# Optimization experiments

Measured on AMD Instinct MI355X. Metric: run time of the kernel, lower is better.

Reference implementation:

```python
import jax, jax.numpy as jnp
import numpy as np

NUM_HEADS = 16
MAX_LEN = 2048


def setup_inputs() -> dict:
    key = jax.random.key(0)
    ks = jax.random.split(key, 10)
    L, B, C = 2048, 2, 1024
    s = 0.02
    return {
        "x": jax.random.normal(ks[0], (L, B, C), dtype=jnp.float32),
        "Wq": jax.random.normal(ks[1], (C, C), dtype=jnp.float32) * s,
        "bq": jnp.zeros((C,), dtype=jnp.float32),
        "Wk": jax.random.normal(ks[2], (C, C), dtype=jnp.float32) * s,
        "bk": jnp.zeros((C,), dtype=jnp.float32),
        "Wv": jax.random.normal(ks[3], (C, C), dtype=jnp.float32) * s,
        "bv": jnp.zeros((C,), dtype=jnp.float32),
        "Wo": jax.random.normal(ks[4], (C, C), dtype=jnp.float32) * s,
        "bo": jnp.zeros((C,), dtype=jnp.float32),
        "rel": jax.random.normal(ks[5], (2 * MAX_LEN - 1,), dtype=jnp.float32) * s,
    }


def reference(x, Wq, bq, Wk, bk, Wv, bv, Wo, bo, rel):
    L, B, C = x.shape
    H = NUM_HEADS
    hd = C // H
    scale = hd ** (-0.5)
    xb = jnp.transpose(x, (1, 0, 2))  # (B, L, C)

    def heads(y):  # (B, L, C) -> (B, H, L, hd)
        return jnp.transpose(y.reshape(B, L, H, hd), (0, 2, 1, 3))

    Q = heads(xb @ Wq + bq)
    K = heads(xb @ Wk + bk)
    V = heads(xb @ Wv + bv)

    scores = jnp.einsum("bhqd,bhkd->bhqk", Q, K)  # (B, H, L, L)
    # relative-position bias gather: offset = k - q + max_len - 1
    idx = jnp.arange(L)[None, :] - jnp.arange(L)[:, None] + (MAX_LEN - 1)
    R = rel[idx]  # (L, L)
    scores = (scores + R[None, None, :, :]) * scale
    w = jax.nn.softmax(scores, axis=-1)
    attn = jnp.einsum("bhqk,bhkd->bhqd", w, V)  # (B, H, L, hd)
    attn = jnp.transpose(attn, (0, 2, 1, 3)).reshape(B, L, C)
    attn = jnp.transpose(attn, (1, 0, 2))  # (L, B, C)
    return attn @ Wo + bo
```

## Files before the change

kernel.cpp:

```cpp
#include <hip/hip_runtime.h>

#define L_SEQ 2048
#define BATCH 2
#define CDIM  1024
#define NH    16
#define HD    64

typedef __attribute__((ext_vector_type(8))) short short8;
typedef __attribute__((ext_vector_type(4))) float floatx4;

#define QSCALE 0.18033688011112042f

__device__ __forceinline__ unsigned short f2bf(float f){
  unsigned int u = __builtin_bit_cast(unsigned int, f);
  u += 0x7fffu + ((u >> 16) & 1u);
  return (unsigned short)(u >> 16);
}

__device__ __forceinline__ void gload_lds16(const void* g, void* l){
  typedef __attribute__((address_space(1))) void gv_t;
  typedef __attribute__((address_space(3))) void sv_t;
  __builtin_amdgcn_global_load_lds((gv_t*)(void*)g, (sv_t*)l, 16, 0, 0);
}

__global__ void __launch_bounds__(256) prep_x(const float* __restrict__ x,
                                              unsigned short* __restrict__ xb){
  int idx = blockIdx.x * 256 + threadIdx.x;
  int c4 = idx & 255;
  int lb = idx >> 8;
  int b  = lb & (BATCH - 1);
  int l  = lb >> 1;
  float4 v = ((const float4*)x)[idx];
  ushort4 s;
  s.x = f2bf(v.x); s.y = f2bf(v.y); s.z = f2bf(v.z); s.w = f2bf(v.w);
  *(ushort4*)&xb[(size_t)(b*L_SEQ + l)*CDIM + c4*4] = s;
}

__global__ void __launch_bounds__(256) prep_w(const float* __restrict__ Wq,
    const float* __restrict__ Wk, const float* __restrict__ Wv,
    const float* __restrict__ Wo, unsigned short* __restrict__ Wqkvt,
    unsigned short* __restrict__ Wot){
  __shared__ float tile[32][33];
  int z = blockIdx.z;
  const float* W = (z==0)?Wq:(z==1)?Wk:(z==2)?Wv:Wo;
  unsigned short* dst = (z==3) ? Wot : (Wqkvt + (size_t)z*CDIM*CDIM);
  int tx = threadIdx.x & 31, ty = threadIdx.x >> 5;
  int X = blockIdx.x*32, Y = blockIdx.y*32;
  #pragma unroll
  for (int i=0;i<4;i++)
    tile[ty + i*8][tx] = W[(size_t)(Y + ty + i*8)*CDIM + X + tx];
  __syncthreads();
  #pragma unroll
  for (int i=0;i<4;i++)
    dst[(size_t)(X + ty + i*8)*CDIM + Y + tx] = f2bf(tile[tx][ty + i*8]);
}

template<int MODE>
__global__ void __launch_bounds__(256) gemm_bt(
    const unsigned short* __restrict__ A,
    const unsigned short* __restrict__ Bt,
    int Kdim,
    const float* __restrict__ b0, const float* __restrict__ b1,
    const float* __restrict__ b2,
    unsigned short* __restrict__ qo, unsigned short* __restrict__ ko,
    unsigned short* __restrict__ vo, float* __restrict__ out)
{
  __shared__ unsigned short Asm[128*32];
  __shared__ unsigned short Bsm[128*32];
  const int t    = threadIdx.x;
  const int lane = t & 63;
  const int wave = t >> 6;
  const int wr = wave >> 1, wc = wave & 1;
  const int g = lane >> 4, lr = lane & 15;
  const int rowA0 = blockIdx.x * 128;
  const int rowB0 = blockIdx.y * 128;

  floatx4 acc[4][4] = {};

  const int r_st = t >> 2;
  const int k_st = (t & 3) * 8;

  for (int k0 = 0; k0 < Kdim; k0 += 32) {
    const unsigned short* ga = A  + (size_t)(rowA0 + r_st) * Kdim + k0 + k_st;
    const unsigned short* gb = Bt + (size_t)(rowB0 + r_st) * Kdim + k0 + k_st;
    gload_lds16(ga,                   &Asm[t*8]);
    gload_lds16(ga + (size_t)64*Kdim, &Asm[2048 + t*8]);
    gload_lds16(gb,                   &Bsm[t*8]);
    gload_lds16(gb + (size_t)64*Kdim, &Bsm[2048 + t*8]);
    __syncthreads();
    short8 af[4], bfr[4];
    #pragma unroll
    for (int mi=0;mi<4;mi++)
      af[mi] = *(const short8*)&Asm[(wr*64 + mi*16 + lr)*32 + g*8];
    #pragma unroll
    for (int ni=0;ni<4;ni++)
      bfr[ni] = *(const short8*)&Bsm[(wc*64 + ni*16 + lr)*32 + g*8];
    #pragma unroll
    for (int mi=0;mi<4;mi++)
      #pragma unroll
      for (int ni=0;ni<4;ni++)
        acc[mi][ni] = __builtin_amdgcn_mfma_f32_16x16x32_bf16(af[mi], bfr[ni], acc[mi][ni], 0, 0, 0);
    __syncthreads();
  }

  #pragma unroll
  for (int mi=0;mi<4;mi++){
    const int rb = rowA0 + wr*64 + mi*16 + g*4;
    #pragma unroll
    for (int ni=0;ni<4;ni++){
      const int col = rowB0 + wc*64 + ni*16 + lr;
      if (MODE == 0) {
        const int sec = col >> 10;
        const int nl  = col & 1023;
        const int h = nl >> 6, d = nl & 63;
        const float* bp = (sec==0) ? b0 : (sec==1) ? b1 : b2;
        const float bias = bp[nl];
        #pragma unroll
        for (int r=0;r<4;r++){
          const int row = rb + r;
          const int b = row >> 11, l = row & 2047;
          float v = acc[mi][ni][r] + bias;
          if (sec == 0) v *= QSCALE;
          const unsigned short hv = f2bf(v);
          const size_t bh = (size_t)(b*NH + h);
          if (sec == 0)      qo[(bh*L_SEQ + l)*HD + d] = hv;
          else if (sec == 1) ko[(bh*L_SEQ + l)*HD + d] = hv;
          else               vo[(bh*HD + d)*L_SEQ + l] = hv;
        }
      } else {
        const float bias = b0[col];
        #pragma unroll
        for (int r=0;r<4;r++){
          const int row = rb + r;
          const int b = row >> 11, l = row & 2047;
          out[((size_t)l*BATCH + b)*CDIM + col] = acc[mi][ni][r] + bias;
        }
      }
    }
  }
}

__global__ void __launch_bounds__(256) attn_kernel(
    const unsigned short* __restrict__ Qb, const unsigned short* __restrict__ Kb,
    const unsigned short* __restrict__ Vt, const float* __restrict__ rel,
    unsigned short* __restrict__ Ab)
{
  __shared__ unsigned short Ks[2][64*64];
  __shared__ unsigned short Vs[2][64*64];
  __shared__ unsigned int Pl[4*16*32];
  const int bh = blockIdx.x;
  const int qb = blockIdx.y;
  const int t = threadIdx.x, lane = t & 63, wave = t >> 6;
  const int g = lane >> 4, lr = lane & 15;

  const unsigned short* Qp = Qb + (size_t)bh * (L_SEQ*HD);
  const unsigned short* Kp = Kb + (size_t)bh * (L_SEQ*HD);
  const unsigned short* Vp = Vt + (size_t)bh * (HD*L_SEQ);

  const int q0 = qb*64 + wave*16;
  const short8 qf0 = *(const short8*)&Qp[(size_t)(q0 + lr)*HD + g*8];
  const short8 qf1 = *(const short8*)&Qp[(size_t)(q0 + lr)*HD + 32 + g*8];

  const float* relp = rel + (2047 - q0 - lr + g*4);

  unsigned int* pw = Pl + wave*512 + lr*32;
  const int swz = lr & 7;

  const int srow = t >> 3;
  const int sxor = (t & 7) ^ (srow & 7);

  const unsigned short* kg = Kp + (size_t)srow*HD + sxor*8;
  const unsigned short* vg = Vp + (size_t)srow*L_SEQ + sxor*8;

  floatx4 o[4] = {};
  float m = -1e30f, lsum = 0.f;

  gload_lds16(kg,           &Ks[0][t*8]);
  gload_lds16(kg + 32*HD,   &Ks[0][2048 + t*8]);
  gload_lds16(vg,           &Vs[0][t*8]);
  gload_lds16(vg + (size_t)32*L_SEQ, &Vs[0][2048 + t*8]);
  __syncthreads();

  int cur = 0;
  for (int kb = 0; kb < L_SEQ; kb += 64) {
    {
      const int kbn = (kb + 64) & (L_SEQ - 1);
      const unsigned short* kgn = kg + (size_t)kbn*HD;
      const unsigned short* vgn = vg + kbn;
      unsigned short* kd = &Ks[cur^1][0];
      unsigned short* vd = &Vs[cur^1][0];
      gload_lds16(kgn,                    kd + t*8);
      gload_lds16(kgn + 32*HD,            kd + 2048 + t*8);
      gload_lds16(vgn,                    vd + t*8);
      gload_lds16(vgn + (size_t)32*L_SEQ, vd + 2048 + t*8);
    }

    float relv[16];
    #pragma unroll
    for (int j=0;j<4;j++)
      #pragma unroll
      for (int r=0;r<4;r++)
        relv[4*j+r] = relp[kb + 16*j + r];

    const unsigned short* kbuf = &Ks[cur][0];
    floatx4 s[4];
    #pragma unroll
    for (int j=0;j<4;j++){
      const int row = j*16 + lr;
      const short8 k0 = *(const short8*)&kbuf[row*64 + ((g    ) ^ swz)*8];
      const short8 k1 = *(const short8*)&kbuf[row*64 + ((4 + g) ^ swz)*8];
      floatx4 z = {};
      z = __builtin_amdgcn_mfma_f32_16x16x32_bf16(k0, qf0, z, 0,0,0);
      z = __builtin_amdgcn_mfma_f32_16x16x32_bf16(k1, qf1, z, 0,0,0);
      s[j] = z;
    }

    float p[16];
    #pragma unroll
    for (int j=0;j<4;j++)
      #pragma unroll
      for (int r=0;r<4;r++)
        p[4*j+r] = fmaf(relv[4*j+r], QSCALE, s[j][r]);

    float ma = fmaxf(fmaxf(fmaxf(p[0],p[1]),fmaxf(p[2],p[3])),
                     fmaxf(fmaxf(p[4],p[5]),fmaxf(p[6],p[7])));
    float mb = fmaxf(fmaxf(fmaxf(p[8],p[9]),fmaxf(p[10],p[11])),
                     fmaxf(fmaxf(p[12],p[13]),fmaxf(p[14],p[15])));
    float mx = fmaxf(ma, mb);
    mx = fmaxf(mx, __shfl_xor(mx, 16, 64));
    mx = fmaxf(mx, __shfl_xor(mx, 32, 64));
    const float mn = fmaxf(m, mx);
    const float al = exp2f(m - mn);
    m = mn;
    #pragma unroll
    for (int i=0;i<16;i++) p[i] = exp2f(p[i] - mn);
    float t0 = (p[0]+p[1]) + (p[2]+p[3]);
    float t1 = (p[4]+p[5]) + (p[6]+p[7]);
    float t2 = (p[8]+p[9]) + (p[10]+p[11]);
    float t3 = (p[12]+p[13]) + (p[14]+p[15]);
    float ss = (t0+t1) + (t2+t3);
    ss += __shfl_xor(ss, 16, 64);
    ss += __shfl_xor(ss, 32, 64);
    lsum = lsum*al + ss;
    #pragma unroll
    for (int fb=0;fb<4;fb++)
      #pragma unroll
      for (int r=0;r<4;r++) o[fb][r] *= al;

    #pragma unroll
    for (int j=0;j<4;j++){
      unsigned lo = (unsigned)f2bf(p[4*j])   | ((unsigned)f2bf(p[4*j+1])<<16);
      unsigned hi = (unsigned)f2bf(p[4*j+2]) | ((unsigned)f2bf(p[4*j+3])<<16);
      const int unit = (2*j + (g>>1)) ^ swz;
      *(uint2*)&pw[unit*4 + (g&1)*2] = make_uint2(lo, hi);
    }
    asm volatile("" ::: "memory");
    const short8 pf0 = *(const short8*)&pw[((    g) ^ swz)*4];
    const short8 pf1 = *(const short8*)&pw[((4 + g) ^ swz)*4];
    asm volatile("" ::: "memory");

    const unsigned short* vbuf = &Vs[cur][0];
    #pragma unroll
    for (int fb=0; fb<4; fb++){
      const int row = fb*16 + lr;
      const short8 v0 = *(const short8*)&vbuf[row*64 + ((g    ) ^ swz)*8];
      const short8 v1 = *(const short8*)&vbuf[row*64 + ((4 + g) ^ swz)*8];
      o[fb] = __builtin_amdgcn_mfma_f32_16x16x32_bf16(v0, pf0, o[fb], 0,0,0);
      o[fb] = __builtin_amdgcn_mfma_f32_16x16x32_bf16(v1, pf1, o[fb], 0,0,0);
    }

    __syncthreads();
    cur ^= 1;
  }

  const float inv = 1.f / lsum;
  const int b = bh >> 4, h = bh & 15;
  unsigned short* outp = &Ab[((size_t)(b*L_SEQ + q0 + lr))*CDIM + h*HD];
  #pragma unroll
  for (int fb=0; fb<4; fb++){
    #pragma unroll
    for (int rp=0; rp<2; rp++){
      const float v0 = o[fb][2*rp]   * inv;
      const float v1 = o[fb][2*rp+1] * inv;
      *(unsigned int*)&outp[fb*16 + g*4 + 2*rp] =
          (unsigned)f2bf(v0) | ((unsigned)f2bf(v1) << 16);
    }
  }
}

extern "C" void kernel_launch(void* const* d_in, const int* in_sizes, int n_in,
                              void* d_out, int out_size, void* d_ws, size_t ws_size,
                              hipStream_t stream) {
  const float* x   = (const float*)d_in[0];
  const float* Wq  = (const float*)d_in[1];
  const float* bq  = (const float*)d_in[2];
  const float* Wk  = (const float*)d_in[3];
  const float* bk  = (const float*)d_in[4];
  const float* Wv  = (const float*)d_in[5];
  const float* bv  = (const float*)d_in[6];
  const float* Wo  = (const float*)d_in[7];
  const float* bo  = (const float*)d_in[8];
  const float* rel = (const float*)d_in[9];
  float* out = (float*)d_out;

  char* ws = (char*)d_ws;
  unsigned short* Xb    = (unsigned short*)(ws);
  unsigned short* Wqkvt = (unsigned short*)(ws + (8u  << 20));
  unsigned short* Wot   = (unsigned short*)(ws + (14u << 20));
  unsigned short* Qb    = (unsigned short*)(ws + (16u << 20));
  unsigned short* Kb    = (unsigned short*)(ws + (24u << 20));
  unsigned short* Vt    = (unsigned short*)(ws + (32u << 20));
  unsigned short* Ab    = Xb;

  prep_x<<<4096, 256, 0, stream>>>(x, Xb);
  prep_w<<<dim3(32,32,4), 256, 0, stream>>>(Wq, Wk, Wv, Wo, Wqkvt, Wot);
  gemm_bt<0><<<dim3(32,24), 256, 0, stream>>>(Xb, Wqkvt, CDIM, bq, bk, bv,
                                              Qb, Kb, Vt, nullptr);
  attn_kernel<<<dim3(32,32), 256, 0, stream>>>(Qb, Kb, Vt, rel, Ab);
  gemm_bt<1><<<dim3(32,8), 256, 0, stream>>>(Ab, Wot, CDIM, bo, nullptr, nullptr,
                                             nullptr, nullptr, nullptr, out);
}
```

Measured before the change: 248.8 us.

## Lazy softmax rescale, MFMA row-sum, and packed bf16 conversion in attention

The online-softmax running max is now updated only when some lane's block max exceeds the stored max by more than a threshold of 8 (in log2 units), so the cross-lane max shuffles and output rescaling are skipped on most iterations. The row-sum reduction is moved onto the matrix cores by multiplying a ones vector with the bf16 probability fragments, which removes the shuffle-based sum. Manual bf16 rounding is replaced with the hardware packed convert instruction. The trade-off is extra MFMA work per iteration, a divergent branch, and a sum taken over bf16-rounded probabilities that can reach up to 2^8 before rescaling.

```diff
diff --git a/kernel.cpp b/kernel.cpp
--- a/kernel.cpp
+++ b/kernel.cpp
@@ -15,6 +15,12 @@
   unsigned int u = __builtin_bit_cast(unsigned int, f);
   u += 0x7fffu + ((u >> 16) & 1u);
   return (unsigned short)(u >> 16);
+}
+
+__device__ __forceinline__ unsigned cvtpk(float lo, float hi){
+  unsigned r;
+  asm("v_cvt_pk_bf16_f32 %0, %1, %2" : "=v"(r) : "v"(lo), "v"(hi));
+  return r;
 }
 
 __device__ __forceinline__ void gload_lds16(const void* g, void* l){
@@ -166,6 +172,9 @@
   unsigned int* pw = Pl + wave*512 + lr*32;
   const int swz = lr & 7;
 
+  const short ONE = (short)0x3F80;
+  const short8 ones = { ONE,ONE,ONE,ONE,ONE,ONE,ONE,ONE };
+
   const int srow = t >> 3;
   const int sxor = (t & 7) ^ (srow & 7);
 
@@ -173,7 +182,8 @@
   const unsigned short* vg = Vp + (size_t)srow*L_SEQ + sxor*8;
 
   floatx4 o[4] = {};
-  float m = -1e30f, lsum = 0.f;
+  floatx4 osum = {};
+  float m = -1e30f;
 
   gload_lds16(kg,           &Ks[0][t*8]);
   gload_lds16(kg + 32*HD,   &Ks[0][2048 + t*8]);
@@ -222,35 +232,32 @@
       for (int r=0;r<4;r++)
         p[4*j+r] = fmaf(relv[4*j+r], QSCALE, s[j][r]);
 
-    float ma = fmaxf(fmaxf(fmaxf(p[0],p[1]),fmaxf(p[2],p[3])),
-                     fmaxf(fmaxf(p[4],p[5]),fmaxf(p[6],p[7])));
-    float mb = fmaxf(fmaxf(fmaxf(p[8],p[9]),fmaxf(p[10],p[11])),
-                     fmaxf(fmaxf(p[12],p[13]),fmaxf(p[14],p[15])));
-    float mx = fmaxf(ma, mb);
-    mx = fmaxf(mx, __shfl_xor(mx, 16, 64));
-    mx = fmaxf(mx, __shfl_xor(mx, 32, 64));
-    const float mn = fmaxf(m, mx);
-    const float al = exp2f(m - mn);
-    m = mn;
-    #pragma unroll
-    for (int i=0;i<16;i++) p[i] = exp2f(p[i] - mn);
-    float t0 = (p[0]+p[1]) + (p[2]+p[3]);
-    float t1 = (p[4]+p[5]) + (p[6]+p[7]);
-    float t2 = (p[8]+p[9]) + (p[10]+p[11]);
-    float t3 = (p[12]+p[13]) + (p[14]+p[15]);
-    float ss = (t0+t1) + (t2+t3);
-    ss += __shfl_xor(ss, 16, 64);
-    ss += __shfl_xor(ss, 32, 64);
-    lsum = lsum*al + ss;
-    #pragma unroll
-    for (int fb=0;fb<4;fb++)
-      #pragma unroll
-      for (int r=0;r<4;r++) o[fb][r] *= al;
+    float ma = fmaxf(fmaxf(fmaxf(p[0],p[1]),p[2]),  fmaxf(fmaxf(p[3],p[4]),p[5]));
+    float mb = fmaxf(fmaxf(fmaxf(p[6],p[7]),p[8]),  fmaxf(fmaxf(p[9],p[10]),p[11]));
+    float mc = fmaxf(fmaxf(fmaxf(p[12],p[13]),p[14]), p[15]);
+    float mxl = fmaxf(fmaxf(ma, mb), mc);
+
+    if (!__all(mxl <= m + 8.f)) {
+      float mx = fmaxf(mxl, __shfl_xor(mxl, 16, 64));
+      mx = fmaxf(mx, __shfl_xor(mx, 32, 64));
+      const float mn = fmaxf(m, mx);
+      const float al = exp2f(m - mn);
+      m = mn;
+      #pragma unroll
+      for (int r=0;r<4;r++) osum[r] *= al;
+      #pragma unroll
+      for (int fb=0;fb<4;fb++)
+        #pragma unroll
+        for (int r=0;r<4;r++) o[fb][r] *= al;
+    }
+
+    #pragma unroll
+    for (int i=0;i<16;i++) p[i] = exp2f(p[i] - m);
 
     #pragma unroll
     for (int j=0;j<4;j++){
-      unsigned lo = (unsigned)f2bf(p[4*j])   | ((unsigned)f2bf(p[4*j+1])<<16);
-      unsigned hi = (unsigned)f2bf(p[4*j+2]) | ((unsigned)f2bf(p[4*j+3])<<16);
+      unsigned lo = cvtpk(p[4*j],   p[4*j+1]);
+      unsigned hi = cvtpk(p[4*j+2], p[4*j+3]);
       const int unit = (2*j + (g>>1)) ^ swz;
       *(uint2*)&pw[unit*4 + (g&1)*2] = make_uint2(lo, hi);
     }
@@ -258,6 +265,9 @@
     const short8 pf0 = *(const short8*)&pw[((    g) ^ swz)*4];
     const short8 pf1 = *(const short8*)&pw[((4 + g) ^ swz)*4];
     asm volatile("" ::: "memory");
+
+    osum = __builtin_amdgcn_mfma_f32_16x16x32_bf16(ones, pf0, osum, 0,0,0);
+    osum = __builtin_amdgcn_mfma_f32_16x16x32_bf16(ones, pf1, osum, 0,0,0);
 
     const unsigned short* vbuf = &Vs[cur][0];
     #pragma unroll
@@ -273,17 +283,15 @@
     cur ^= 1;
   }
 
-  const float inv = 1.f / lsum;
+  const float inv = 1.f / osum[0];
   const int b = bh >> 4, h = bh & 15;
   unsigned short* outp = &Ab[((size_t)(b*L_SEQ + q0 + lr))*CDIM + h*HD];
   #pragma unroll
   for (int fb=0; fb<4; fb++){
     #pragma unroll
     for (int rp=0; rp<2; rp++){
-      const float v0 = o[fb][2*rp]   * inv;
-      const float v1 = o[fb][2*rp+1] * inv;
       *(unsigned int*)&outp[fb*16 + g*4 + 2*rp] =
-          (unsigned)f2bf(v0) | ((unsigned)f2bf(v1) << 16);
+          cvtpk(o[fb][2*rp] * inv, o[fb][2*rp+1] * inv);
     }
   }
 }
```

After: 240.3 us. -3.4%, faster.
